# Kernel tuning notes

Hardware: AMD Instinct MI355X
Metric: run time of the kernel (lower is better)

Reference implementation:

```python
import jax, jax.numpy as jnp
import numpy as np

B, T, F, CI, CO, K, DIL = 16, 512, 32, 128, 128, 3, 2


def setup_inputs() -> dict:
    key = jax.random.key(0)
    k1, k2, k3 = jax.random.split(key, 3)
    x = jax.random.normal(k1, (B, T, F, CI), dtype=jnp.float32)
    # torch Conv1d weight per feature: [CO, CI, K]; stack over features -> [F, CO, CI, K]
    fan_in = CI * K
    bound = 1.0 / np.sqrt(fan_in)
    w = jax.random.uniform(k2, (F, CO, CI, K), dtype=jnp.float32, minval=-bound, maxval=bound)
    b = jax.random.uniform(k3, (F, CO), dtype=jnp.float32, minval=-bound, maxval=bound)
    return {"x": x, "w": w, "b": b}


def reference(x, w, b):
    # Causal dilated conv, independent filters per feature.
    left_pad = DIL * (K - 1)
    xpad = jnp.pad(x, ((0, 0), (left_pad, 0), (0, 0), (0, 0)))  # [B, T+L, F, CI]
    # taps[k] = xpad[:, k*DIL : k*DIL + T] -> stack over kernel taps: [K, B, T, F, CI]
    taps = jnp.stack([xpad[:, k * DIL:k * DIL + T] for k in range(K)], axis=0)
    # y[b,t,f,o] = sum_{k,i} taps[k,b,t,f,i] * w[f,o,i,k] + b[f,o]
    y = jnp.einsum('kbtfi,foik->btfo', taps, w) + b[None, None, :, :]
    return y  # dropout p=0.0 (eval) is identity
```

## Files before the change

### kernel.cpp

```cpp
#include <hip/hip_runtime.h>
#include <stdint.h>

#define B_ 16
#define T_ 512
#define F_ 32
#define CI_ 128
#define CO_ 128
#define K_ 3
#define LPAD 4
#define TM 128
#define XROWS (TM + LPAD)
#define PITCH 136
#define WT_TILE (CO_ * PITCH)

typedef __attribute__((ext_vector_type(8))) __bf16 bf16x8;
typedef __attribute__((ext_vector_type(4))) float f32x4;

__device__ __forceinline__ uint16_t f2bf(float x) {
  uint32_t u = __builtin_bit_cast(uint32_t, x);
  u += 0x7fffu + ((u >> 16) & 1u);
  return (uint16_t)(u >> 16);
}

__global__ __launch_bounds__(256) void repack_w(const float* __restrict__ w,
                                                uint16_t* __restrict__ wt) {
  int idx = blockIdx.x * 256 + threadIdx.x;
  int c4 = idx % 34;
  int rest = idx / 34;
  int o = rest & (CO_ - 1);
  rest >>= 7;
  int k = rest % 3;
  int f = rest / 3;
  if (f >= F_) return;
  uint16_t h[4];
#pragma unroll
  for (int j = 0; j < 4; ++j) {
    int i = c4 * 4 + j;
    float v = (i < CI_) ? w[(((size_t)(f * CO_ + o)) * CI_ + i) * K_ + k] : 0.f;
    h[j] = f2bf(v);
  }
  uint2 pk;
  pk.x = (uint32_t)h[0] | ((uint32_t)h[1] << 16);
  pk.y = (uint32_t)h[2] | ((uint32_t)h[3] << 16);
  *(uint2*)&wt[((size_t)(f * 3 + k) * CO_ + o) * PITCH + c4 * 4] = pk;
}

template <bool PACKED>
__global__ __launch_bounds__(256, 2) void conv_main(
    const float* __restrict__ x, const uint16_t* __restrict__ wt,
    const float* __restrict__ wraw, const float* __restrict__ bias,
    float* __restrict__ y) {
  __shared__ __align__(16) uint16_t xs[XROWS * PITCH];
  __shared__ __align__(16) uint16_t wsm[CO_ * PITCH];

  const int bid = blockIdx.x;
  const int f = bid >> 6;
  const int mt = bid & 63;
  const int b = mt >> 2;
  const int t0 = (mt & 3) << 7;

  const int tid = threadIdx.x;
  const int lane = tid & 63;
  const int wave = tid >> 6;
  const int wm = wave >> 1;
  const int wn = wave & 1;
  const int l15 = lane & 15;
  const int quad = lane >> 4;

  f32x4 acc[4][4];
#pragma unroll
  for (int fn = 0; fn < 4; ++fn) {
    float bv = bias[f * CO_ + wn * 64 + fn * 16 + l15];
#pragma unroll
    for (int fm = 0; fm < 4; ++fm) acc[fm][fn] = (f32x4){bv, bv, bv, bv};
  }

  {
    const float* xb = x + ((size_t)b * T_ * F_ + f) * CI_;
    for (int idx = tid; idx < XROWS * 32; idx += 256) {
      int row = idx >> 5, c4 = idx & 31;
      int t = t0 - LPAD + row;
      float4 v = make_float4(0.f, 0.f, 0.f, 0.f);
      if (t >= 0) v = *(const float4*)(xb + (size_t)t * (F_ * CI_) + c4 * 4);
      uint2 pk;
      pk.x = (uint32_t)f2bf(v.x) | ((uint32_t)f2bf(v.y) << 16);
      pk.y = (uint32_t)f2bf(v.z) | ((uint32_t)f2bf(v.w) << 16);
      *(uint2*)&xs[row * PITCH + c4 * 4] = pk;
    }
  }

#pragma unroll 1
  for (int k = 0; k < K_; ++k) {
    if constexpr (PACKED) {
      const uint16_t* wk = wt + (size_t)(f * 3 + k) * WT_TILE;
      for (int c = wave; c < 34; c += 4) {
        __builtin_amdgcn_global_load_lds(
            (const __attribute__((address_space(1))) uint32_t*)(wk + c * 512 + lane * 8),
            (__attribute__((address_space(3))) uint32_t*)&wsm[c * 512], 16, 0, 0);
      }
    } else {
      for (int idx = tid; idx < CO_ * 32; idx += 256) {
        int o = idx >> 5, c4 = idx & 31;
        const float* ws0 = wraw + (((size_t)(f * CO_ + o)) * CI_ + c4 * 4) * K_ + k;
        uint2 pk;
        pk.x = (uint32_t)f2bf(ws0[0]) | ((uint32_t)f2bf(ws0[3]) << 16);
        pk.y = (uint32_t)f2bf(ws0[6]) | ((uint32_t)f2bf(ws0[9]) << 16);
        *(uint2*)&wsm[o * PITCH + c4 * 4] = pk;
      }
    }
    __syncthreads();

    const int xr0 = wm * 64 + l15 + 2 * k;
    const int wr0 = wn * 64 + l15;
    const int kq = quad * 8;
#pragma unroll
    for (int i0 = 0; i0 < CI_; i0 += 32) {
      bf16x8 av[4], bv[4];
#pragma unroll
      for (int fm = 0; fm < 4; ++fm)
        av[fm] = *(const bf16x8*)&xs[(xr0 + fm * 16) * PITCH + i0 + kq];
#pragma unroll
      for (int fn = 0; fn < 4; ++fn)
        bv[fn] = *(const bf16x8*)&wsm[(wr0 + fn * 16) * PITCH + i0 + kq];
#pragma unroll
      for (int fm = 0; fm < 4; ++fm)
#pragma unroll
        for (int fn = 0; fn < 4; ++fn)
          acc[fm][fn] = __builtin_amdgcn_mfma_f32_16x16x32_bf16(av[fm], bv[fn],
                                                                acc[fm][fn], 0, 0, 0);
    }
    if (k < K_ - 1) __syncthreads();
  }

  float* yb = y + ((size_t)b * T_ * F_ + f) * CO_;
#pragma unroll
  for (int fm = 0; fm < 4; ++fm) {
    int r0 = t0 + wm * 64 + fm * 16 + quad * 4;
#pragma unroll
    for (int fn = 0; fn < 4; ++fn) {
      int col = wn * 64 + fn * 16 + l15;
#pragma unroll
      for (int r = 0; r < 4; ++r)
        yb[(size_t)(r0 + r) * (F_ * CO_) + col] = acc[fm][fn][r];
    }
  }
}

extern "C" void kernel_launch(void* const* d_in, const int* in_sizes, int n_in,
                              void* d_out, int out_size, void* d_ws, size_t ws_size,
                              hipStream_t stream) {
  const float* x = (const float*)d_in[0];
  const float* w = (const float*)d_in[1];
  const float* bias = (const float*)d_in[2];
  float* y = (float*)d_out;

  const size_t wt_bytes = (size_t)F_ * 3 * WT_TILE * sizeof(uint16_t);
  const int main_blocks = F_ * B_ * (T_ / TM);

  if (ws_size >= wt_bytes) {
    uint16_t* wtp = (uint16_t*)d_ws;
    const int total = F_ * 3 * CO_ * 34;
    repack_w<<<(total + 255) / 256, 256, 0, stream>>>(w, wtp);
    conv_main<true><<<main_blocks, 256, 0, stream>>>(x, wtp, w, bias, y);
  } else {
    conv_main<false><<<main_blocks, 256, 0, stream>>>(x, (const uint16_t*)nullptr, w, bias, y);
  }
}
```

Measured before the change: 308.2 us.

## Halve time tile and double-buffer weight chunks in LDS with async loads

Cuts the time tile from 128 to 64 rows and splits the weights into 12 chunks of 32 input channels, one set per tap. Each chunk is prefetched into a second LDS buffer with global_load_lds while the current one feeds the MFMAs. The repack kernel now writes this chunked layout with one thread per (f,o,i) reading all three taps. The aim is to hide weight-load latency and raise occupancy (launch bounds 4) through the smaller LDS footprint and fewer accumulators. The cost is twice as many blocks, each reloading all weights and the x halo, plus 12 barriers per block instead of 3.

```diff
diff --git a/kernel.cpp b/kernel.cpp
--- a/kernel.cpp
+++ b/kernel.cpp
@@ -8,10 +8,12 @@
 #define CO_ 128
 #define K_ 3
 #define LPAD 4
-#define TM 128
+#define TM 64
 #define XROWS (TM + LPAD)
-#define PITCH 136
-#define WT_TILE (CO_ * PITCH)
+#define XPITCH 136
+#define WPITCH 32
+#define CHUNK_ELEMS (CO_ * WPITCH)
+#define NCHUNK 12
 
 typedef __attribute__((ext_vector_type(8))) __bf16 bf16x8;
 typedef __attribute__((ext_vector_type(4))) float f32x4;
@@ -23,41 +25,33 @@
 }
 
 __global__ __launch_bounds__(256) void repack_w(const float* __restrict__ w,
-                                                uint16_t* __restrict__ wt) {
+                                                uint16_t* __restrict__ wt2) {
   int idx = blockIdx.x * 256 + threadIdx.x;
-  int c4 = idx % 34;
-  int rest = idx / 34;
-  int o = rest & (CO_ - 1);
-  rest >>= 7;
-  int k = rest % 3;
-  int f = rest / 3;
-  if (f >= F_) return;
-  uint16_t h[4];
-#pragma unroll
-  for (int j = 0; j < 4; ++j) {
-    int i = c4 * 4 + j;
-    float v = (i < CI_) ? w[(((size_t)(f * CO_ + o)) * CI_ + i) * K_ + k] : 0.f;
-    h[j] = f2bf(v);
-  }
-  uint2 pk;
-  pk.x = (uint32_t)h[0] | ((uint32_t)h[1] << 16);
-  pk.y = (uint32_t)h[2] | ((uint32_t)h[3] << 16);
-  *(uint2*)&wt[((size_t)(f * 3 + k) * CO_ + o) * PITCH + c4 * 4] = pk;
+  int i = idx & (CI_ - 1);
+  int fo = idx >> 7;
+  int o = fo & (CO_ - 1);
+  int f = fo >> 7;
+  const float* src = w + (size_t)idx * K_;
+  float a0 = src[0], a1 = src[1], a2 = src[2];
+  size_t base = ((size_t)f * NCHUNK + (i >> 5)) * CHUNK_ELEMS + o * WPITCH + (i & 31);
+  wt2[base] = f2bf(a0);
+  wt2[base + 4 * (size_t)CHUNK_ELEMS] = f2bf(a1);
+  wt2[base + 8 * (size_t)CHUNK_ELEMS] = f2bf(a2);
 }
 
 template <bool PACKED>
-__global__ __launch_bounds__(256, 2) void conv_main(
-    const float* __restrict__ x, const uint16_t* __restrict__ wt,
+__global__ __launch_bounds__(256, 4) void conv_main(
+    const float* __restrict__ x, const uint16_t* __restrict__ wt2,
     const float* __restrict__ wraw, const float* __restrict__ bias,
     float* __restrict__ y) {
-  __shared__ __align__(16) uint16_t xs[XROWS * PITCH];
-  __shared__ __align__(16) uint16_t wsm[CO_ * PITCH];
+  __shared__ __align__(16) uint16_t xs[XROWS * XPITCH];
+  __shared__ __align__(16) uint16_t wbuf[2][CHUNK_ELEMS];
 
   const int bid = blockIdx.x;
-  const int f = bid >> 6;
-  const int mt = bid & 63;
-  const int b = mt >> 2;
-  const int t0 = (mt & 3) << 7;
+  const int f = bid >> 7;
+  const int mt = bid & 127;
+  const int b = mt >> 3;
+  const int t0 = (mt & 7) << 6;
 
   const int tid = threadIdx.x;
   const int lane = tid & 63;
@@ -67,13 +61,30 @@
   const int l15 = lane & 15;
   const int quad = lane >> 4;
 
-  f32x4 acc[4][4];
+  f32x4 acc[2][4];
 #pragma unroll
   for (int fn = 0; fn < 4; ++fn) {
     float bv = bias[f * CO_ + wn * 64 + fn * 16 + l15];
 #pragma unroll
-    for (int fm = 0; fm < 4; ++fm) acc[fm][fn] = (f32x4){bv, bv, bv, bv};
+    for (int fm = 0; fm < 2; ++fm) acc[fm][fn] = (f32x4){bv, bv, bv, bv};
   }
+
+  auto issue_chunk = [&](int idx, int buf) {
+    const uint16_t* src = wt2 + ((size_t)(f * NCHUNK + idx)) * CHUNK_ELEMS;
+    for (int c = wave; c < 8; c += 4)
+      __builtin_amdgcn_global_load_lds(
+          (const __attribute__((address_space(1))) uint32_t*)(src + c * 512 + lane * 8),
+          (__attribute__((address_space(3))) uint32_t*)&wbuf[buf][c * 512], 16, 0, 0);
+  };
+  auto gather_chunk = [&](int idx, int buf) {
+    int tap = idx >> 2, i0 = (idx & 3) << 5;
+    for (int e = tid; e < CHUNK_ELEMS; e += 256) {
+      int o = e >> 5, i = i0 + (e & 31);
+      wbuf[buf][e] = f2bf(wraw[(((size_t)(f * CO_ + o)) * CI_ + i) * K_ + tap]);
+    }
+  };
+
+  if constexpr (PACKED) issue_chunk(0, 0);
 
   {
     const float* xb = x + ((size_t)b * T_ * F_ + f) * CI_;
@@ -85,57 +96,43 @@
       uint2 pk;
       pk.x = (uint32_t)f2bf(v.x) | ((uint32_t)f2bf(v.y) << 16);
       pk.y = (uint32_t)f2bf(v.z) | ((uint32_t)f2bf(v.w) << 16);
-      *(uint2*)&xs[row * PITCH + c4 * 4] = pk;
+      *(uint2*)&xs[row * XPITCH + c4 * 4] = pk;
     }
   }
+  if constexpr (!PACKED) gather_chunk(0, 0);
+  __syncthreads();
 
 #pragma unroll 1
-  for (int k = 0; k < K_; ++k) {
-    if constexpr (PACKED) {
-      const uint16_t* wk = wt + (size_t)(f * 3 + k) * WT_TILE;
-      for (int c = wave; c < 34; c += 4) {
-        __builtin_amdgcn_global_load_lds(
-            (const __attribute__((address_space(1))) uint32_t*)(wk + c * 512 + lane * 8),
-            (__attribute__((address_space(3))) uint32_t*)&wsm[c * 512], 16, 0, 0);
-      }
-    } else {
-      for (int idx = tid; idx < CO_ * 32; idx += 256) {
-        int o = idx >> 5, c4 = idx & 31;
-        const float* ws0 = wraw + (((size_t)(f * CO_ + o)) * CI_ + c4 * 4) * K_ + k;
-        uint2 pk;
-        pk.x = (uint32_t)f2bf(ws0[0]) | ((uint32_t)f2bf(ws0[3]) << 16);
-        pk.y = (uint32_t)f2bf(ws0[6]) | ((uint32_t)f2bf(ws0[9]) << 16);
-        *(uint2*)&wsm[o * PITCH + c4 * 4] = pk;
-      }
+  for (int idx = 0; idx < NCHUNK; ++idx) {
+    const int cur = idx & 1;
+    if (idx + 1 < NCHUNK) {
+      if constexpr (PACKED) issue_chunk(idx + 1, cur ^ 1);
+      else gather_chunk(idx + 1, cur ^ 1);
     }
-    __syncthreads();
 
-    const int xr0 = wm * 64 + l15 + 2 * k;
-    const int wr0 = wn * 64 + l15;
-    const int kq = quad * 8;
+    const int tap = idx >> 2;
+    const int kq0 = (idx & 3) * 32 + quad * 8;
+    const int xr0 = wm * 32 + l15 + 2 * tap;
+    bf16x8 av[2], bv[4];
 #pragma unroll
-    for (int i0 = 0; i0 < CI_; i0 += 32) {
-      bf16x8 av[4], bv[4];
+    for (int fm = 0; fm < 2; ++fm)
+      av[fm] = *(const bf16x8*)&xs[(xr0 + fm * 16) * XPITCH + kq0];
 #pragma unroll
-      for (int fm = 0; fm < 4; ++fm)
-        av[fm] = *(const bf16x8*)&xs[(xr0 + fm * 16) * PITCH + i0 + kq];
+    for (int fn = 0; fn < 4; ++fn)
+      bv[fn] = *(const bf16x8*)&wbuf[cur][(wn * 64 + fn * 16 + l15) * WPITCH + quad * 8];
+#pragma unroll
+    for (int fm = 0; fm < 2; ++fm)
 #pragma unroll
       for (int fn = 0; fn < 4; ++fn)
-        bv[fn] = *(const bf16x8*)&wsm[(wr0 + fn * 16) * PITCH + i0 + kq];
-#pragma unroll
-      for (int fm = 0; fm < 4; ++fm)
-#pragma unroll
-        for (int fn = 0; fn < 4; ++fn)
-          acc[fm][fn] = __builtin_amdgcn_mfma_f32_16x16x32_bf16(av[fm], bv[fn],
-                                                                acc[fm][fn], 0, 0, 0);
-    }
-    if (k < K_ - 1) __syncthreads();
+        acc[fm][fn] = __builtin_amdgcn_mfma_f32_16x16x32_bf16(av[fm], bv[fn],
+                                                              acc[fm][fn], 0, 0, 0);
+    if (idx + 1 < NCHUNK) __syncthreads();
   }
 
   float* yb = y + ((size_t)b * T_ * F_ + f) * CO_;
 #pragma unroll
-  for (int fm = 0; fm < 4; ++fm) {
-    int r0 = t0 + wm * 64 + fm * 16 + quad * 4;
+  for (int fm = 0; fm < 2; ++fm) {
+    int r0 = t0 + wm * 32 + fm * 16 + quad * 4;
 #pragma unroll
     for (int fn = 0; fn < 4; ++fn) {
       int col = wn * 64 + fn * 16 + l15;
@@ -154,14 +151,14 @@
   const float* bias = (const float*)d_in[2];
   float* y = (float*)d_out;
 
-  const size_t wt_bytes = (size_t)F_ * 3 * WT_TILE * sizeof(uint16_t);
+  const size_t wt2_bytes = (size_t)F_ * NCHUNK * CHUNK_ELEMS * sizeof(uint16_t);
   const int main_blocks = F_ * B_ * (T_ / TM);
 
-  if (ws_size >= wt_bytes) {
-    uint16_t* wtp = (uint16_t*)d_ws;
-    const int total = F_ * 3 * CO_ * 34;
-    repack_w<<<(total + 255) / 256, 256, 0, stream>>>(w, wtp);
-    conv_main<true><<<main_blocks, 256, 0, stream>>>(x, wtp, w, bias, y);
+  if (ws_size >= wt2_bytes) {
+    uint16_t* wt2 = (uint16_t*)d_ws;
+    const int total = F_ * CO_ * CI_;
+    repack_w<<<total / 256, 256, 0, stream>>>(w, wt2);
+    conv_main<true><<<main_blocks, 256, 0, stream>>>(x, wt2, w, bias, y);
   } else {
     conv_main<false><<<main_blocks, 256, 0, stream>>>(x, (const uint16_t*)nullptr, w, bias, y);
   }
```

Measured after the change: 278.9 us. -9.5%, faster.
